# Optimization experiments

Hardware: AMD Instinct MI355X
Metric: run time of the kernel (lower is better)

## Reference

```python
import jax, jax.numpy as jnp
import numpy as np

LOG2 = float(np.log(2.0))

def ssp(x):
    # shifted softplus used throughout SchNet
    return jax.nn.softplus(x) - LOG2

def setup_inputs() -> dict:
    key = jax.random.key(0)
    ks = jax.random.split(key, 12)
    B, Na, Nn, G, F = 16, 512, 64, 25, 128
    s = 0.05
    return {
        "x": jax.random.normal(ks[0], (B, Na, F), jnp.float32),
        "r_ij": jax.random.uniform(ks[1], (B, Na, Nn), jnp.float32),
        "f_ij": jax.random.uniform(ks[2], (B, Na, Nn, G), jnp.float32),
        "neighbours": jax.random.randint(ks[3], (B, Na, Nn), 0, Na),
        "pairwise_mask": jax.random.uniform(ks[4], (B, Na, Nn), jnp.float32),
        "W_in2f": jax.random.normal(ks[5], (F, F), jnp.float32) * s,
        "W_f1": jax.random.normal(ks[6], (G, F), jnp.float32) * s,
        "b_f1": jnp.zeros((F,), jnp.float32),
        "W_f2": jax.random.normal(ks[7], (F, F), jnp.float32) * s,
        "b_f2": jnp.zeros((F,), jnp.float32),
        "W_out": jax.random.normal(ks[8], (F, F), jnp.float32) * s,
        "b_out": jnp.zeros((F,), jnp.float32),
    }

def reference(x, r_ij, f_ij, neighbours, pairwise_mask,
              W_in2f, W_f1, b_f1, W_f2, b_f2, W_out, b_out):
    # filter_network: Dense(G->F, ssp) -> Dense(F->F)
    W = jnp.einsum('bang,gf->banf', f_ij, W_f1) + b_f1  # [B,Na,Nn,F]
    W = ssp(W)
    W = jnp.einsum('banf,fg->bang', W, W_f2) + b_f2
    # in2f (no bias)
    y = jnp.einsum('bai,if->baf', x, W_in2f)  # [B,Na,F]
    B, Na, Nn = neighbours.shape
    # gather neighbor features: y[b, neighbours[b,a,n], :]
    nbh = neighbours.reshape(B, Na * Nn, 1)
    g = jnp.take_along_axis(y, nbh, axis=1).reshape(B, Na, Nn, -1)
    # filter multiply, mask, aggregate over neighbor axis (sum, no mean)
    agg = jnp.sum(g * W * pairwise_mask[..., None], axis=2)  # [B,Na,F]
    # f2out with shifted softplus activation
    out = ssp(jnp.einsum('baf,fo->bao', agg, W_out) + b_out)
    return out
```

## Files before the change

kernel.cpp:

```cpp
#include <hip/hip_runtime.h>

typedef __attribute__((ext_vector_type(8))) short bf16x8;
typedef __attribute__((ext_vector_type(4))) float f32x4;
typedef __attribute__((ext_vector_type(4))) unsigned int u32x4;

#define LOG2F 0.69314718055994531f
#define LOG2EF 1.4426950408889634f

#define NB 16
#define NA 512
#define NN 64
#define NG 25
#define NF 128

__device__ __forceinline__ unsigned short f2bf(float x) {
    __bf16 h = (__bf16)x;
    return __builtin_bit_cast(unsigned short, h);
}
__device__ __forceinline__ float ssp2(float s) {
    float t = __builtin_amdgcn_exp2f(s);
    return fmaf(__builtin_amdgcn_logf(1.0f + t), LOG2F, -LOG2F);
}

#define FRAG_WF1 0
#define FRAG_WF2 4096
#define FRAG_WIN 20480
#define FRAG_WOUT 36864
#define B1S_OFF   106496
#define YBF_OFF   107008
#define AGG_OFF   2204160

__global__ __launch_bounds__(256) void k_prep(
    const float* __restrict__ Wf1, const float* __restrict__ Wf2,
    const float* __restrict__ Win, const float* __restrict__ Wout,
    const float* __restrict__ b1, char* __restrict__ ws)
{
    unsigned short* frag = (unsigned short*)ws;
    int idx = blockIdx.x * 256 + threadIdx.x;
    if (idx < 4096) {
        int j = idx & 7, lane = (idx >> 3) & 63, tc = idx >> 9;
        int f1 = tc * 16 + (lane & 15);
        int g  = (lane >> 4) * 8 + j;
        frag[idx] = (g < NG) ? f2bf(Wf1[g * NF + f1] * LOG2EF) : (unsigned short)0;
    } else if (idx < 20480) {
        int t = idx - 4096;
        int j = t & 7, lane = (t >> 3) & 63, ks = (t >> 9) & 3, tn = t >> 11;
        int f = tn * 16 + (lane & 15);
        int k = ks * 32 + (lane >> 4) * 8 + j;
        frag[idx] = f2bf(Wf2[k * NF + f]);
    } else if (idx < 36864) {
        int t = idx - 20480;
        int j = t & 7, lane = (t >> 3) & 63, ks = (t >> 9) & 3, tn = t >> 11;
        int f = tn * 16 + (lane & 15);
        int k = ks * 32 + (lane >> 4) * 8 + j;
        frag[idx] = f2bf(Win[k * NF + f]);
    } else if (idx < 53248) {
        int t = idx - 36864;
        int j = t & 7, lane = (t >> 3) & 63, ks = (t >> 9) & 3, tn = t >> 11;
        int f = tn * 16 + (lane & 15);
        int k = ks * 32 + (lane >> 4) * 8 + j;
        frag[idx] = f2bf(Wout[k * NF + f]);
    } else if (idx < 53376) {
        ((float*)(ws + B1S_OFF))[idx - 53248] = b1[idx - 53248] * LOG2EF;
    }
}

__global__ __launch_bounds__(256) void k_in2f(
    const float* __restrict__ x, const unsigned short* __restrict__ frag,
    unsigned short* __restrict__ ybf)
{
    const unsigned short* winfrag = frag + FRAG_WIN;
    const int lane = threadIdx.x & 63, w = threadIdx.x >> 6;
    const int rowbase = blockIdx.x * 32;
    f32x4 acc[2][2];
    f32x4 z = {0.f, 0.f, 0.f, 0.f};
    acc[0][0] = z; acc[0][1] = z; acc[1][0] = z; acc[1][1] = z;
#pragma unroll
    for (int ks = 0; ks < 4; ++ks) {
        bf16x8 a[2];
#pragma unroll
        for (int tm = 0; tm < 2; ++tm) {
            int row = rowbase + tm * 16 + (lane & 15);
            int k0  = ks * 32 + (lane >> 4) * 8;
            const float* p = x + (size_t)row * NF + k0;
            float4 v0 = *(const float4*)p;
            float4 v1 = *(const float4*)(p + 4);
            bf16x8 t;
            t[0] = (short)f2bf(v0.x); t[1] = (short)f2bf(v0.y);
            t[2] = (short)f2bf(v0.z); t[3] = (short)f2bf(v0.w);
            t[4] = (short)f2bf(v1.x); t[5] = (short)f2bf(v1.y);
            t[6] = (short)f2bf(v1.z); t[7] = (short)f2bf(v1.w);
            a[tm] = t;
        }
#pragma unroll
        for (int tn = 0; tn < 2; ++tn) {
            bf16x8 bfr = *(const bf16x8*)(winfrag + ((((w * 2 + tn) * 4 + ks) * 64) + lane) * 8);
#pragma unroll
            for (int tm = 0; tm < 2; ++tm)
                acc[tm][tn] = __builtin_amdgcn_mfma_f32_16x16x32_bf16(a[tm], bfr, acc[tm][tn], 0, 0, 0);
        }
    }
#pragma unroll
    for (int tm = 0; tm < 2; ++tm)
#pragma unroll
        for (int tn = 0; tn < 2; ++tn)
#pragma unroll
            for (int r = 0; r < 4; ++r) {
                int row = rowbase + tm * 16 + (lane >> 4) * 4 + r;
                int f   = w * 32 + tn * 16 + (lane & 15);
                ybf[(size_t)row * NF + f] = f2bf(acc[tm][tn][r]);
            }
}

__global__ __launch_bounds__(256, 6) void k_cfconv(
    const float* __restrict__ fij, const int* __restrict__ nbh,
    const float* __restrict__ mask, const float* __restrict__ b1s,
    const float* __restrict__ b2, const unsigned short* __restrict__ frag,
    const unsigned short* __restrict__ ybf, float* __restrict__ agg)
{
    __shared__ alignas(16) char smem[16896];
    float* sfij          = (float*)smem;
    unsigned short* sW1T = (unsigned short*)smem;
    float* smask         = (float*)(smem + 16384);
    int*   snbh          = (int*)(smem + 16640);

    const int tid = threadIdx.x, lane = tid & 63, w = tid >> 6;
    const int g = lane >> 4, lc = lane & 15;
    const int atom = blockIdx.x;
    const int bidx = atom >> 9;
    const int fbase = w * 32;
    const int fc0 = fbase + lc;

    if (tid < 64) {
        smask[tid] = mask[(size_t)atom * NN + tid];
        snbh[tid]  = nbh[(size_t)atom * NN + tid];
    }

    {
        const char* fb = (const char*)(fij + (size_t)atom * (NN * NG));
        __builtin_amdgcn_global_load_lds(
            (const __attribute__((address_space(1))) void*)(fb + w * 1024 + lane * 16),
            (__attribute__((address_space(3))) void*)((char*)sfij + w * 1024), 16, 0, 0);
        if (w < 2) {
            __builtin_amdgcn_global_load_lds(
                (const __attribute__((address_space(1))) void*)(fb + (w + 4) * 1024 + lane * 16),
                (__attribute__((address_space(3))) void*)((char*)sfij + (w + 4) * 1024), 16, 0, 0);
        }
        if (w == 3) {
            __builtin_amdgcn_global_load_lds(
                (const __attribute__((address_space(1))) void*)(fb + 6144 + lane * 4),
                (__attribute__((address_space(3))) void*)((char*)sfij + 6144), 4, 0, 0);
        }
    }

    const unsigned short* wf1frag = frag + FRAG_WF1;
    bf16x8 afr[2], vb[4];
    f32x4  rg[8];
#pragma unroll
    for (int i = 0; i < 2; ++i)
        afr[i] = *(const bf16x8*)(wf1frag + (((2 * w + i) * 64) + lane) * 8);

    __syncthreads();

    {
        const int g0 = g * 8;
        const unsigned int m0 = (g == 3) ? 0x0000FFFFu : 0xFFFFFFFFu;
        const unsigned int m1 = (g == 3) ? 0u : 0xFFFFFFFFu;
#pragma unroll
        for (int tn = 0; tn < 4; ++tn) {
            int n = tn * 16 + lc;
            const float* p = sfij + n * NG + g0;
            bf16x8 t;
            t[0] = (short)f2bf(p[0]); t[1] = (short)f2bf(p[1]);
            t[2] = (short)f2bf(p[2]); t[3] = (short)f2bf(p[3]);
            t[4] = (short)f2bf(p[4]); t[5] = (short)f2bf(p[5]);
            t[6] = (short)f2bf(p[6]); t[7] = (short)f2bf(p[7]);
            u32x4 tv = __builtin_bit_cast(u32x4, t);
            tv[0] &= m0; tv[1] &= m1; tv[2] &= m1; tv[3] &= m1;
            vb[tn] = __builtin_bit_cast(bf16x8, tv);
        }
    }

    __syncthreads();

#pragma unroll
    for (int i = 0; i < 2; ++i) {
        int c0 = (2 * w + i) * 16 + g * 4;
        f32x4 ci = *(const f32x4*)(b1s + c0);
#pragma unroll
        for (int tn = 0; tn < 4; ++tn)
            rg[i * 4 + tn] = __builtin_amdgcn_mfma_f32_16x16x32_bf16(afr[i], vb[tn], ci, 0, 0, 0);
    }

#pragma unroll
    for (int i = 0; i < 2; ++i) {
        int c0 = (2 * w + i) * 16 + g * 4;
#pragma unroll
        for (int tn = 0; tn < 4; ++tn) {
            int n = tn * 16 + lc;
            ushort4 pk;
#pragma unroll
            for (int r = 0; r < 4; ++r)
                ((unsigned short*)&pk)[r] = f2bf(ssp2(rg[i * 4 + tn][r]));
            *(ushort4*)((char*)sW1T + n * 256 + ((c0 * 2) ^ ((n & 7) << 4))) = pk;
        }
    }
    __syncthreads();

    const unsigned short* wf2frag = frag + FRAG_WF2;
    const float bias0 = b2[fc0], bias1 = b2[fc0 + 16];
#pragma unroll
    for (int tm = 0; tm < 4; ++tm) {
        rg[tm * 2 + 0] = f32x4{bias0, bias0, bias0, bias0};
        rg[tm * 2 + 1] = f32x4{bias1, bias1, bias1, bias1};
    }
#pragma unroll
    for (int ks = 0; ks < 4; ++ks) {
#pragma unroll
        for (int tm = 0; tm < 4; ++tm) {
            int n  = tm * 16 + lc;
            int kb = ks * 64 + g * 16;
            vb[tm] = *(const bf16x8*)((char*)sW1T + n * 256 + (kb ^ ((n & 7) << 4)));
        }
#pragma unroll
        for (int tnl = 0; tnl < 2; ++tnl) {
            int tn = w * 2 + tnl;
            bf16x8 bf2 = *(const bf16x8*)(wf2frag + (((tn * 4 + ks) * 64) + lane) * 8);
#pragma unroll
            for (int tm = 0; tm < 4; ++tm)
                rg[tm * 2 + tnl] = __builtin_amdgcn_mfma_f32_16x16x32_bf16(vb[tm], bf2, rg[tm * 2 + tnl], 0, 0, 0);
        }
    }

    float aggv0 = 0.f, aggv1 = 0.f;
    const unsigned short* yb = ybf + (size_t)bidx * NA * NF;
#pragma unroll
    for (int tm = 0; tm < 4; ++tm) {
        f32x4 m4 = *(const f32x4*)(smask + tm * 16 + g * 4);
        int4  nb4 = *(const int4*)(snbh + tm * 16 + g * 4);
#pragma unroll
        for (int r = 0; r < 4; ++r) {
            int yrow = (r == 0) ? nb4.x : (r == 1) ? nb4.y : (r == 2) ? nb4.z : nb4.w;
            const unsigned short* yp = yb + (size_t)yrow * NF + fc0;
            float y0 = __builtin_bit_cast(float, (unsigned int)yp[0] << 16);
            float y1 = __builtin_bit_cast(float, (unsigned int)yp[16] << 16);
            aggv0 = fmaf(rg[tm * 2 + 0][r] * m4[r], y0, aggv0);
            aggv1 = fmaf(rg[tm * 2 + 1][r] * m4[r], y1, aggv1);
        }
    }
    aggv0 += __shfl_xor(aggv0, 16); aggv1 += __shfl_xor(aggv1, 16);
    aggv0 += __shfl_xor(aggv0, 32); aggv1 += __shfl_xor(aggv1, 32);
    if (lane < 16) {
        float* ap = agg + (size_t)atom * NF + fbase;
        ap[lane] = aggv0;
        ap[16 + lane] = aggv1;
    }
}

__global__ __launch_bounds__(256) void k_out(
    const float* __restrict__ agg, const unsigned short* __restrict__ frag,
    const float* __restrict__ bout, float* __restrict__ out)
{
    const unsigned short* wofrag = frag + FRAG_WOUT;
    const int lane = threadIdx.x & 63, w = threadIdx.x >> 6;
    const int rowbase = blockIdx.x * 32;
    const int f0 = w * 32 + (lane & 15);
    const float bo0 = bout[f0], bo1 = bout[f0 + 16];
    f32x4 acc[2][2];
    acc[0][0] = f32x4{bo0, bo0, bo0, bo0};
    acc[1][0] = f32x4{bo0, bo0, bo0, bo0};
    acc[0][1] = f32x4{bo1, bo1, bo1, bo1};
    acc[1][1] = f32x4{bo1, bo1, bo1, bo1};
#pragma unroll
    for (int ks = 0; ks < 4; ++ks) {
        bf16x8 a[2];
#pragma unroll
        for (int tm = 0; tm < 2; ++tm) {
            int row = rowbase + tm * 16 + (lane & 15);
            int k0  = ks * 32 + (lane >> 4) * 8;
            const float* p = agg + (size_t)row * NF + k0;
            float4 v0 = *(const float4*)p;
            float4 v1 = *(const float4*)(p + 4);
            bf16x8 t;
            t[0] = (short)f2bf(v0.x); t[1] = (short)f2bf(v0.y);
            t[2] = (short)f2bf(v0.z); t[3] = (short)f2bf(v0.w);
            t[4] = (short)f2bf(v1.x); t[5] = (short)f2bf(v1.y);
            t[6] = (short)f2bf(v1.z); t[7] = (short)f2bf(v1.w);
            a[tm] = t;
        }
#pragma unroll
        for (int tn = 0; tn < 2; ++tn) {
            bf16x8 bfr = *(const bf16x8*)(wofrag + ((((w * 2 + tn) * 4 + ks) * 64) + lane) * 8);
#pragma unroll
            for (int tm = 0; tm < 2; ++tm)
                acc[tm][tn] = __builtin_amdgcn_mfma_f32_16x16x32_bf16(a[tm], bfr, acc[tm][tn], 0, 0, 0);
        }
    }
    float lg2 = LOG2EF;
#pragma unroll
    for (int tm = 0; tm < 2; ++tm)
#pragma unroll
        for (int tn = 0; tn < 2; ++tn)
#pragma unroll
            for (int r = 0; r < 4; ++r) {
                int row = rowbase + tm * 16 + (lane >> 4) * 4 + r;
                int f   = w * 32 + tn * 16 + (lane & 15);
                out[(size_t)row * NF + f] = ssp2(acc[tm][tn][r] * lg2);
            }
}

extern "C" void kernel_launch(void* const* d_in, const int* in_sizes, int n_in,
                              void* d_out, int out_size, void* d_ws, size_t ws_size,
                              hipStream_t stream)
{
    (void)in_sizes; (void)n_in; (void)out_size; (void)ws_size;
    const float* x    = (const float*)d_in[0];
    const float* fij  = (const float*)d_in[2];
    const int*   nbh  = (const int*)d_in[3];
    const float* mask = (const float*)d_in[4];
    const float* Win  = (const float*)d_in[5];
    const float* Wf1  = (const float*)d_in[6];
    const float* b1   = (const float*)d_in[7];
    const float* Wf2  = (const float*)d_in[8];
    const float* b2   = (const float*)d_in[9];
    const float* Wout = (const float*)d_in[10];
    const float* bout = (const float*)d_in[11];
    float* out = (float*)d_out;

    char* ws = (char*)d_ws;
    unsigned short* frag = (unsigned short*)ws;
    const float*    b1s  = (const float*)(ws + B1S_OFF);
    unsigned short* ybf  = (unsigned short*)(ws + YBF_OFF);
    float*          agg  = (float*)(ws + AGG_OFF);

    k_prep  <<<209,  256, 0, stream>>>(Wf1, Wf2, Win, Wout, b1, ws);
    k_in2f  <<<256,  256, 0, stream>>>(x, frag, ybf);
    k_cfconv<<<8192, 256, 0, stream>>>(fij, nbh, mask, b1s, b2, frag, ybf, agg);
    k_out   <<<256,  256, 0, stream>>>(agg, frag, bout, out);
}
```

Baseline: 59.38 us.

## Process two atoms per cfconv block and prefetch next atom's f_ij during compute

Each k_cfconv block now handles two consecutive atoms, halving the grid. The second atom's f_ij tile is staged into a separate LDS buffer while the first atom's filter network runs, and per-block constants (W_f1 fragments, biases) are loaded once and reused. The separate sfij and sW1T buffers enlarge LDS use, and the occupancy hint drops from 6 to 4 blocks per CU, so there is less parallelism to hide latency.

Measured after the change: 59.49 us. About the same (+0.2%).

```diff
diff --git a/kernel.cpp b/kernel.cpp
--- a/kernel.cpp
+++ b/kernel.cpp
@@ -20,6 +20,23 @@
 __device__ __forceinline__ float ssp2(float s) {
     float t = __builtin_amdgcn_exp2f(s);
     return fmaf(__builtin_amdgcn_logf(1.0f + t), LOG2F, -LOG2F);
+}
+
+__device__ __forceinline__ void stage_fij(const float* fp, float* sfij, int w, int lane) {
+    const char* fb = (const char*)fp;
+    __builtin_amdgcn_global_load_lds(
+        (const __attribute__((address_space(1))) void*)(fb + w * 1024 + lane * 16),
+        (__attribute__((address_space(3))) void*)((char*)sfij + w * 1024), 16, 0, 0);
+    if (w < 2) {
+        __builtin_amdgcn_global_load_lds(
+            (const __attribute__((address_space(1))) void*)(fb + (w + 4) * 1024 + lane * 16),
+            (__attribute__((address_space(3))) void*)((char*)sfij + (w + 4) * 1024), 16, 0, 0);
+    }
+    if (w == 3) {
+        __builtin_amdgcn_global_load_lds(
+            (const __attribute__((address_space(1))) void*)(fb + 6144 + lane * 4),
+            (__attribute__((address_space(3))) void*)((char*)sfij + 6144), 4, 0, 0);
+    }
 }
 
 #define FRAG_WF1 0
@@ -112,148 +129,145 @@
             }
 }
 
-__global__ __launch_bounds__(256, 6) void k_cfconv(
+__global__ __launch_bounds__(256, 4) void k_cfconv(
     const float* __restrict__ fij, const int* __restrict__ nbh,
     const float* __restrict__ mask, const float* __restrict__ b1s,
     const float* __restrict__ b2, const unsigned short* __restrict__ frag,
     const unsigned short* __restrict__ ybf, float* __restrict__ agg)
 {
-    __shared__ alignas(16) char smem[16896];
-    float* sfij          = (float*)smem;
-    unsigned short* sW1T = (unsigned short*)smem;
-    float* smask         = (float*)(smem + 16384);
-    int*   snbh          = (int*)(smem + 16640);
+    __shared__ alignas(16) float sfij[1600];
+    __shared__ alignas(16) unsigned short sW1T[8192];
+    __shared__ alignas(16) float smask[128];
+    __shared__ alignas(16) int   snbh[128];
 
     const int tid = threadIdx.x, lane = tid & 63, w = tid >> 6;
     const int g = lane >> 4, lc = lane & 15;
-    const int atom = blockIdx.x;
-    const int bidx = atom >> 9;
+    const int a0 = blockIdx.x * 2;
+    const int bidx = a0 >> 9;
     const int fbase = w * 32;
     const int fc0 = fbase + lc;
 
-    if (tid < 64) {
-        smask[tid] = mask[(size_t)atom * NN + tid];
-        snbh[tid]  = nbh[(size_t)atom * NN + tid];
-    }
-
-    {
-        const char* fb = (const char*)(fij + (size_t)atom * (NN * NG));
-        __builtin_amdgcn_global_load_lds(
-            (const __attribute__((address_space(1))) void*)(fb + w * 1024 + lane * 16),
-            (__attribute__((address_space(3))) void*)((char*)sfij + w * 1024), 16, 0, 0);
-        if (w < 2) {
-            __builtin_amdgcn_global_load_lds(
-                (const __attribute__((address_space(1))) void*)(fb + (w + 4) * 1024 + lane * 16),
-                (__attribute__((address_space(3))) void*)((char*)sfij + (w + 4) * 1024), 16, 0, 0);
-        }
-        if (w == 3) {
-            __builtin_amdgcn_global_load_lds(
-                (const __attribute__((address_space(1))) void*)(fb + 6144 + lane * 4),
-                (__attribute__((address_space(3))) void*)((char*)sfij + 6144), 4, 0, 0);
-        }
-    }
+    if (tid < 128) {
+        smask[tid] = mask[(size_t)a0 * NN + tid];
+        snbh[tid]  = nbh[(size_t)a0 * NN + tid];
+    }
+
+    stage_fij(fij + (size_t)a0 * (NN * NG), sfij, w, lane);
 
     const unsigned short* wf1frag = frag + FRAG_WF1;
+    const unsigned short* wf2frag = frag + FRAG_WF2;
     bf16x8 afr[2], vb[4];
     f32x4  rg[8];
 #pragma unroll
     for (int i = 0; i < 2; ++i)
         afr[i] = *(const bf16x8*)(wf1frag + (((2 * w + i) * 64) + lane) * 8);
+    f32x4 ci[2];
+#pragma unroll
+    for (int i = 0; i < 2; ++i)
+        ci[i] = *(const f32x4*)(b1s + (2 * w + i) * 16 + g * 4);
+    const float bias0 = b2[fc0], bias1 = b2[fc0 + 16];
+    const unsigned short* yb = ybf + (size_t)bidx * NA * NF;
 
     __syncthreads();
 
-    {
-        const int g0 = g * 8;
-        const unsigned int m0 = (g == 3) ? 0x0000FFFFu : 0xFFFFFFFFu;
-        const unsigned int m1 = (g == 3) ? 0u : 0xFFFFFFFFu;
-#pragma unroll
-        for (int tn = 0; tn < 4; ++tn) {
-            int n = tn * 16 + lc;
-            const float* p = sfij + n * NG + g0;
-            bf16x8 t;
-            t[0] = (short)f2bf(p[0]); t[1] = (short)f2bf(p[1]);
-            t[2] = (short)f2bf(p[2]); t[3] = (short)f2bf(p[3]);
-            t[4] = (short)f2bf(p[4]); t[5] = (short)f2bf(p[5]);
-            t[6] = (short)f2bf(p[6]); t[7] = (short)f2bf(p[7]);
-            u32x4 tv = __builtin_bit_cast(u32x4, t);
-            tv[0] &= m0; tv[1] &= m1; tv[2] &= m1; tv[3] &= m1;
-            vb[tn] = __builtin_bit_cast(bf16x8, tv);
-        }
-    }
-
-    __syncthreads();
-
-#pragma unroll
-    for (int i = 0; i < 2; ++i) {
-        int c0 = (2 * w + i) * 16 + g * 4;
-        f32x4 ci = *(const f32x4*)(b1s + c0);
-#pragma unroll
-        for (int tn = 0; tn < 4; ++tn)
-            rg[i * 4 + tn] = __builtin_amdgcn_mfma_f32_16x16x32_bf16(afr[i], vb[tn], ci, 0, 0, 0);
-    }
-
-#pragma unroll
-    for (int i = 0; i < 2; ++i) {
-        int c0 = (2 * w + i) * 16 + g * 4;
-#pragma unroll
-        for (int tn = 0; tn < 4; ++tn) {
-            int n = tn * 16 + lc;
-            ushort4 pk;
-#pragma unroll
-            for (int r = 0; r < 4; ++r)
-                ((unsigned short*)&pk)[r] = f2bf(ssp2(rg[i * 4 + tn][r]));
-            *(ushort4*)((char*)sW1T + n * 256 + ((c0 * 2) ^ ((n & 7) << 4))) = pk;
-        }
-    }
-    __syncthreads();
-
-    const unsigned short* wf2frag = frag + FRAG_WF2;
-    const float bias0 = b2[fc0], bias1 = b2[fc0 + 16];
-#pragma unroll
-    for (int tm = 0; tm < 4; ++tm) {
-        rg[tm * 2 + 0] = f32x4{bias0, bias0, bias0, bias0};
-        rg[tm * 2 + 1] = f32x4{bias1, bias1, bias1, bias1};
-    }
-#pragma unroll
-    for (int ks = 0; ks < 4; ++ks) {
+#pragma unroll
+    for (int a = 0; a < 2; ++a) {
+        {
+            const int g0 = g * 8;
+            const unsigned int m0 = (g == 3) ? 0x0000FFFFu : 0xFFFFFFFFu;
+            const unsigned int m1 = (g == 3) ? 0u : 0xFFFFFFFFu;
+#pragma unroll
+            for (int tn = 0; tn < 4; ++tn) {
+                int n = tn * 16 + lc;
+                const float* p = sfij + n * NG + g0;
+                bf16x8 t;
+                t[0] = (short)f2bf(p[0]); t[1] = (short)f2bf(p[1]);
+                t[2] = (short)f2bf(p[2]); t[3] = (short)f2bf(p[3]);
+                t[4] = (short)f2bf(p[4]); t[5] = (short)f2bf(p[5]);
+                t[6] = (short)f2bf(p[6]); t[7] = (short)f2bf(p[7]);
+                u32x4 tv = __builtin_bit_cast(u32x4, t);
+                tv[0] &= m0; tv[1] &= m1; tv[2] &= m1; tv[3] &= m1;
+                vb[tn] = __builtin_bit_cast(bf16x8, tv);
+            }
+        }
+
+        if (a == 0) {
+            __syncthreads();
+            stage_fij(fij + (size_t)(a0 + 1) * (NN * NG), sfij, w, lane);
+        }
+
+#pragma unroll
+        for (int i = 0; i < 2; ++i)
+#pragma unroll
+            for (int tn = 0; tn < 4; ++tn)
+                rg[i * 4 + tn] = __builtin_amdgcn_mfma_f32_16x16x32_bf16(afr[i], vb[tn], ci[i], 0, 0, 0);
+
+#pragma unroll
+        for (int i = 0; i < 2; ++i) {
+            int c0 = (2 * w + i) * 16 + g * 4;
+#pragma unroll
+            for (int tn = 0; tn < 4; ++tn) {
+                int n = tn * 16 + lc;
+                ushort4 pk;
+#pragma unroll
+                for (int r = 0; r < 4; ++r)
+                    ((unsigned short*)&pk)[r] = f2bf(ssp2(rg[i * 4 + tn][r]));
+                *(ushort4*)((char*)sW1T + n * 256 + ((c0 * 2) ^ ((n & 7) << 4))) = pk;
+            }
+        }
+        __syncthreads();
+
 #pragma unroll
         for (int tm = 0; tm < 4; ++tm) {
-            int n  = tm * 16 + lc;
-            int kb = ks * 64 + g * 16;
-            vb[tm] = *(const bf16x8*)((char*)sW1T + n * 256 + (kb ^ ((n & 7) << 4)));
-        }
-#pragma unroll
-        for (int tnl = 0; tnl < 2; ++tnl) {
-            int tn = w * 2 + tnl;
-            bf16x8 bf2 = *(const bf16x8*)(wf2frag + (((tn * 4 + ks) * 64) + lane) * 8);
-#pragma unroll
-            for (int tm = 0; tm < 4; ++tm)
-                rg[tm * 2 + tnl] = __builtin_amdgcn_mfma_f32_16x16x32_bf16(vb[tm], bf2, rg[tm * 2 + tnl], 0, 0, 0);
-        }
-    }
-
-    float aggv0 = 0.f, aggv1 = 0.f;
-    const unsigned short* yb = ybf + (size_t)bidx * NA * NF;
-#pragma unroll
-    for (int tm = 0; tm < 4; ++tm) {
-        f32x4 m4 = *(const f32x4*)(smask + tm * 16 + g * 4);
-        int4  nb4 = *(const int4*)(snbh + tm * 16 + g * 4);
-#pragma unroll
-        for (int r = 0; r < 4; ++r) {
-            int yrow = (r == 0) ? nb4.x : (r == 1) ? nb4.y : (r == 2) ? nb4.z : nb4.w;
-            const unsigned short* yp = yb + (size_t)yrow * NF + fc0;
-            float y0 = __builtin_bit_cast(float, (unsigned int)yp[0] << 16);
-            float y1 = __builtin_bit_cast(float, (unsigned int)yp[16] << 16);
-            aggv0 = fmaf(rg[tm * 2 + 0][r] * m4[r], y0, aggv0);
-            aggv1 = fmaf(rg[tm * 2 + 1][r] * m4[r], y1, aggv1);
-        }
-    }
-    aggv0 += __shfl_xor(aggv0, 16); aggv1 += __shfl_xor(aggv1, 16);
-    aggv0 += __shfl_xor(aggv0, 32); aggv1 += __shfl_xor(aggv1, 32);
-    if (lane < 16) {
-        float* ap = agg + (size_t)atom * NF + fbase;
-        ap[lane] = aggv0;
-        ap[16 + lane] = aggv1;
+            rg[tm * 2 + 0] = f32x4{bias0, bias0, bias0, bias0};
+            rg[tm * 2 + 1] = f32x4{bias1, bias1, bias1, bias1};
+        }
+#pragma unroll
+        for (int ks = 0; ks < 4; ++ks) {
+#pragma unroll
+            for (int tm = 0; tm < 4; ++tm) {
+                int n  = tm * 16 + lc;
+                int kb = ks * 64 + g * 16;
+                vb[tm] = *(const bf16x8*)((char*)sW1T + n * 256 + (kb ^ ((n & 7) << 4)));
+            }
+#pragma unroll
+            for (int tnl = 0; tnl < 2; ++tnl) {
+                int tn = w * 2 + tnl;
+                bf16x8 bf2 = *(const bf16x8*)(wf2frag + (((tn * 4 + ks) * 64) + lane) * 8);
+#pragma unroll
+                for (int tm = 0; tm < 4; ++tm)
+                    rg[tm * 2 + tnl] = __builtin_amdgcn_mfma_f32_16x16x32_bf16(vb[tm], bf2, rg[tm * 2 + tnl], 0, 0, 0);
+            }
+        }
+
+        {
+            const float* sm = smask + a * 64;
+            const int*   sn = snbh + a * 64;
+            float aggv0 = 0.f, aggv1 = 0.f;
+#pragma unroll
+            for (int tm = 0; tm < 4; ++tm) {
+                f32x4 m4 = *(const f32x4*)(sm + tm * 16 + g * 4);
+                int4  nb4 = *(const int4*)(sn + tm * 16 + g * 4);
+#pragma unroll
+                for (int r = 0; r < 4; ++r) {
+                    int yrow = (r == 0) ? nb4.x : (r == 1) ? nb4.y : (r == 2) ? nb4.z : nb4.w;
+                    const unsigned short* yp = yb + (size_t)yrow * NF + fc0;
+                    float y0 = __builtin_bit_cast(float, (unsigned int)yp[0] << 16);
+                    float y1 = __builtin_bit_cast(float, (unsigned int)yp[16] << 16);
+                    aggv0 = fmaf(rg[tm * 2 + 0][r] * m4[r], y0, aggv0);
+                    aggv1 = fmaf(rg[tm * 2 + 1][r] * m4[r], y1, aggv1);
+                }
+            }
+            aggv0 += __shfl_xor(aggv0, 16); aggv1 += __shfl_xor(aggv1, 16);
+            aggv0 += __shfl_xor(aggv0, 32); aggv1 += __shfl_xor(aggv1, 32);
+            if (lane < 16) {
+                float* ap = agg + (size_t)(a0 + a) * NF + fbase;
+                ap[lane] = aggv0;
+                ap[16 + lane] = aggv1;
+            }
+        }
+
+        if (a == 0) __syncthreads();
     }
 }
 
@@ -335,6 +349,6 @@
 
     k_prep  <<<209,  256, 0, stream>>>(Wf1, Wf2, Win, Wout, b1, ws);
     k_in2f  <<<256,  256, 0, stream>>>(x, frag, ybf);
-    k_cfconv<<<8192, 256, 0, stream>>>(fij, nbh, mask, b1s, b2, frag, ybf, agg);
+    k_cfconv<<<4096, 256, 0, stream>>>(fij, nbh, mask, b1s, b2, frag, ybf, agg);
     k_out   <<<256,  256, 0, stream>>>(agg, frag, bout, out);
 }
```

## Prefetch gathered neighbour rows into LDS asynchronously during filter MLP

Applied to the files above, without the earlier changes.

The neighbour feature gather from ybf is moved out of the final aggregation loop. Each block now issues async global-to-LDS loads of all 64 neighbour rows into a swizzled LDS buffer before the filter-network MFMAs, so the gather latency overlaps that compute. The bias loads are also hoisted earlier. LDS per block roughly doubles and the occupancy hint drops from 6 to 4 blocks, which trades occupancy for the overlap.

After: 61.86 us. 1.04x slower.

```diff
diff --git a/kernel.cpp b/kernel.cpp
--- a/kernel.cpp
+++ b/kernel.cpp
@@ -17,9 +17,30 @@
     __bf16 h = (__bf16)x;
     return __builtin_bit_cast(unsigned short, h);
 }
+__device__ __forceinline__ float bf2f(unsigned short h) {
+    union { unsigned int u; float f; } c; c.u = ((unsigned int)h) << 16;
+    return c.f;
+}
 __device__ __forceinline__ float ssp2(float s) {
     float t = __builtin_amdgcn_exp2f(s);
     return fmaf(__builtin_amdgcn_logf(1.0f + t), LOG2F, -LOG2F);
+}
+
+__device__ __forceinline__ void stage_fij(const float* fp, float* sfij, int w, int lane) {
+    const char* fb = (const char*)fp;
+    __builtin_amdgcn_global_load_lds(
+        (const __attribute__((address_space(1))) void*)(fb + w * 1024 + lane * 16),
+        (__attribute__((address_space(3))) void*)((char*)sfij + w * 1024), 16, 0, 0);
+    if (w < 2) {
+        __builtin_amdgcn_global_load_lds(
+            (const __attribute__((address_space(1))) void*)(fb + (w + 4) * 1024 + lane * 16),
+            (__attribute__((address_space(3))) void*)((char*)sfij + (w + 4) * 1024), 16, 0, 0);
+    }
+    if (w == 3) {
+        __builtin_amdgcn_global_load_lds(
+            (const __attribute__((address_space(1))) void*)(fb + 6144 + lane * 4),
+            (__attribute__((address_space(3))) void*)((char*)sfij + 6144), 4, 0, 0);
+    }
 }
 
 #define FRAG_WF1 0
@@ -112,17 +133,18 @@
             }
 }
 
-__global__ __launch_bounds__(256, 6) void k_cfconv(
+__global__ __launch_bounds__(256, 4) void k_cfconv(
     const float* __restrict__ fij, const int* __restrict__ nbh,
     const float* __restrict__ mask, const float* __restrict__ b1s,
     const float* __restrict__ b2, const unsigned short* __restrict__ frag,
     const unsigned short* __restrict__ ybf, float* __restrict__ agg)
 {
-    __shared__ alignas(16) char smem[16896];
+    __shared__ alignas(16) char smem[33280];
     float* sfij          = (float*)smem;
     unsigned short* sW1T = (unsigned short*)smem;
-    float* smask         = (float*)(smem + 16384);
-    int*   snbh          = (int*)(smem + 16640);
+    unsigned short* yLDS = (unsigned short*)(smem + 16384);
+    float* smask         = (float*)(smem + 32768);
+    int*   snbh          = (int*)(smem + 33024);
 
     const int tid = threadIdx.x, lane = tid & 63, w = tid >> 6;
     const int g = lane >> 4, lc = lane & 15;
@@ -136,29 +158,20 @@
         snbh[tid]  = nbh[(size_t)atom * NN + tid];
     }
 
-    {
-        const char* fb = (const char*)(fij + (size_t)atom * (NN * NG));
-        __builtin_amdgcn_global_load_lds(
-            (const __attribute__((address_space(1))) void*)(fb + w * 1024 + lane * 16),
-            (__attribute__((address_space(3))) void*)((char*)sfij + w * 1024), 16, 0, 0);
-        if (w < 2) {
-            __builtin_amdgcn_global_load_lds(
-                (const __attribute__((address_space(1))) void*)(fb + (w + 4) * 1024 + lane * 16),
-                (__attribute__((address_space(3))) void*)((char*)sfij + (w + 4) * 1024), 16, 0, 0);
-        }
-        if (w == 3) {
-            __builtin_amdgcn_global_load_lds(
-                (const __attribute__((address_space(1))) void*)(fb + 6144 + lane * 4),
-                (__attribute__((address_space(3))) void*)((char*)sfij + 6144), 4, 0, 0);
-        }
-    }
+    stage_fij(fij + (size_t)atom * (NN * NG), sfij, w, lane);
 
     const unsigned short* wf1frag = frag + FRAG_WF1;
+    const unsigned short* wf2frag = frag + FRAG_WF2;
     bf16x8 afr[2], vb[4];
     f32x4  rg[8];
 #pragma unroll
     for (int i = 0; i < 2; ++i)
         afr[i] = *(const bf16x8*)(wf1frag + (((2 * w + i) * 64) + lane) * 8);
+    f32x4 ci[2];
+#pragma unroll
+    for (int i = 0; i < 2; ++i)
+        ci[i] = *(const f32x4*)(b1s + (2 * w + i) * 16 + g * 4);
+    const float bias0 = b2[fc0], bias1 = b2[fc0 + 16];
 
     __syncthreads();
 
@@ -183,14 +196,25 @@
 
     __syncthreads();
 
-#pragma unroll
-    for (int i = 0; i < 2; ++i) {
-        int c0 = (2 * w + i) * 16 + g * 4;
-        f32x4 ci = *(const f32x4*)(b1s + c0);
+    {
+        const unsigned short* yb = ybf + (size_t)bidx * NA * NF;
+#pragma unroll
+        for (int qi = 0; qi < 4; ++qi) {
+            int r0 = w * 16 + qi * 4;
+            int row = r0 + (lane >> 4);
+            int chunk = (lane & 15) ^ (qi << 1);
+            const unsigned short* gp = yb + (size_t)snbh[row] * NF + chunk * 8;
+            __builtin_amdgcn_global_load_lds(
+                (const __attribute__((address_space(1))) void*)gp,
+                (__attribute__((address_space(3))) void*)(yLDS + r0 * NF), 16, 0, 0);
+        }
+    }
+
+#pragma unroll
+    for (int i = 0; i < 2; ++i)
 #pragma unroll
         for (int tn = 0; tn < 4; ++tn)
-            rg[i * 4 + tn] = __builtin_amdgcn_mfma_f32_16x16x32_bf16(afr[i], vb[tn], ci, 0, 0, 0);
-    }
+            rg[i * 4 + tn] = __builtin_amdgcn_mfma_f32_16x16x32_bf16(afr[i], vb[tn], ci[i], 0, 0, 0);
 
 #pragma unroll
     for (int i = 0; i < 2; ++i) {
@@ -207,8 +231,6 @@
     }
     __syncthreads();
 
-    const unsigned short* wf2frag = frag + FRAG_WF2;
-    const float bias0 = b2[fc0], bias1 = b2[fc0 + 16];
 #pragma unroll
     for (int tm = 0; tm < 4; ++tm) {
         rg[tm * 2 + 0] = f32x4{bias0, bias0, bias0, bias0};
@@ -233,19 +255,20 @@
     }
 
     float aggv0 = 0.f, aggv1 = 0.f;
-    const unsigned short* yb = ybf + (size_t)bidx * NA * NF;
-#pragma unroll
-    for (int tm = 0; tm < 4; ++tm) {
-        f32x4 m4 = *(const f32x4*)(smask + tm * 16 + g * 4);
-        int4  nb4 = *(const int4*)(snbh + tm * 16 + g * 4);
-#pragma unroll
-        for (int r = 0; r < 4; ++r) {
-            int yrow = (r == 0) ? nb4.x : (r == 1) ? nb4.y : (r == 2) ? nb4.z : nb4.w;
-            const unsigned short* yp = yb + (size_t)yrow * NF + fc0;
-            float y0 = __builtin_bit_cast(float, (unsigned int)yp[0] << 16);
-            float y1 = __builtin_bit_cast(float, (unsigned int)yp[16] << 16);
-            aggv0 = fmaf(rg[tm * 2 + 0][r] * m4[r], y0, aggv0);
-            aggv1 = fmaf(rg[tm * 2 + 1][r] * m4[r], y1, aggv1);
+    {
+        const char* ybase0 = (const char*)yLDS + g * 1024 + (((64 * w + 2 * lc)) ^ (g << 5));
+        const char* ybase1 = (const char*)yLDS + g * 1024 + (((64 * w + 2 * lc) ^ 32) ^ (g << 5));
+#pragma unroll
+        for (int tm = 0; tm < 4; ++tm) {
+            f32x4 m4 = *(const f32x4*)(smask + tm * 16 + g * 4);
+#pragma unroll
+            for (int r = 0; r < 4; ++r) {
+                int off = (tm * 16 + r) * 256;
+                float y0 = bf2f(*(const unsigned short*)(ybase0 + off));
+                float y1 = bf2f(*(const unsigned short*)(ybase1 + off));
+                aggv0 = fmaf(rg[tm * 2 + 0][r] * m4[r], y0, aggv0);
+                aggv1 = fmaf(rg[tm * 2 + 1][r] * m4[r], y1, aggv1);
+            }
         }
     }
     aggv0 += __shfl_xor(aggv0, 16); aggv1 += __shfl_xor(aggv1, 16);
```
